# Kernel tuning notes

Hardware: AMD Instinct MI355X
Metric: run time of the kernel (lower is better)

The kernel has to match this reference:

```python
import jax, jax.numpy as jnp
import numpy as np

N = 50000       # nodes
E = 800000      # edges (avg degree 16)
HID = 128       # hidden_size
H = 8           # num_heads
DH = HID // H   # head_dim = 16


def setup_inputs() -> dict:
    key = jax.random.key(0)
    ks = jax.random.split(key, 9)
    wscale = (1.0 / HID) ** 0.5  # ~ torch Linear init scale
    inp = {
        "h": jax.random.normal(ks[0], (N, HID), jnp.float32),
        "val": jnp.ones((E,), jnp.float32),          # A.val (adjacency values)
        "Wq": jax.random.normal(ks[1], (HID, HID), jnp.float32) * wscale,
        "bq": jax.random.normal(ks[2], (HID,), jnp.float32) * wscale,
        "Wk": jax.random.normal(ks[3], (HID, HID), jnp.float32) * wscale,
        "bk": jax.random.normal(ks[4], (HID,), jnp.float32) * wscale,
        "Wv": jax.random.normal(ks[5], (HID, HID), jnp.float32) * wscale,
        "bv": jax.random.normal(ks[6], (HID,), jnp.float32) * wscale,
        "src": jax.random.randint(ks[7], (E,), 0, N, jnp.int32),
        "dst": jax.random.randint(ks[8], (E,), 0, N, jnp.int32),
    }
    return inp


def reference(h, val, Wq, bq, Wk, bk, Wv, bv, src, dst):
    scaling = DH ** (-0.5)
    # projections (torch Linear: x @ W.T + b), reshape (N, head_dim, num_heads)
    q = (h @ Wq.T + bq).reshape(N, DH, H) * scaling
    k = (h @ Wk.T + bk).reshape(N, DH, H)
    v = (h @ Wv.T + bv).reshape(N, DH, H)
    # bsddmm: per-edge per-head scores, masked/scaled by adjacency values
    score = jnp.einsum("edh,edh->eh", q[src], k[dst]) * val[:, None]  # [E, H]
    # sparse per-row softmax (stable, segment-wise over src rows)
    m = jax.ops.segment_max(score, src, num_segments=N)               # [N, H]
    p = jnp.exp(score - m[src])
    s = jax.ops.segment_sum(p, src, num_segments=N)                   # [N, H]
    attn = p / s[src]                                                 # [E, H]
    # bspmm: weighted aggregation of v over edges
    out = jax.ops.segment_sum(attn[:, None, :] * v[dst], src, num_segments=N)  # [N, DH, H]
    return out.reshape(N, HID)
```

## Files before the change

kernel.cpp:

```cpp
#include <hip/hip_runtime.h>
#include <hip/hip_bf16.h>
#include <math.h>

#define HID 128
#define NH  8
#define SCHUNK 512
#define TPAD 136

typedef __attribute__((ext_vector_type(8))) short short8;
typedef __attribute__((ext_vector_type(4))) float f32x4;

static __device__ __forceinline__ float blo(unsigned int u) {
  union { unsigned int i; float f; } c; c.i = u << 16; return c.f;
}
static __device__ __forceinline__ float bhi(unsigned int u) {
  union { unsigned int i; float f; } c; c.i = u & 0xFFFF0000u; return c.f;
}
static __device__ __forceinline__ unsigned short f2bf(float f) {
  union { float f; unsigned int i; } c; c.f = f;
  unsigned int r = c.i + 0x7FFFu + ((c.i >> 16) & 1u);
  return (unsigned short)(r >> 16);
}

__global__ void convert_kernel(const float* __restrict__ src,
                               unsigned short* __restrict__ dst, int n8) {
  int stride = gridDim.x * blockDim.x;
  for (int i = blockIdx.x * blockDim.x + threadIdx.x; i < n8; i += stride) {
    float4 a = ((const float4*)src)[2 * i];
    float4 b = ((const float4*)src)[2 * i + 1];
    uint4 o;
    o.x = ((unsigned int)f2bf(a.y) << 16) | f2bf(a.x);
    o.y = ((unsigned int)f2bf(a.w) << 16) | f2bf(a.z);
    o.z = ((unsigned int)f2bf(b.y) << 16) | f2bf(b.x);
    o.w = ((unsigned int)f2bf(b.w) << 16) | f2bf(b.z);
    ((uint4*)dst)[i] = o;
  }
}

__global__ void convert3_kernel(const float* __restrict__ s0, const float* __restrict__ s1,
                                const float* __restrict__ s2,
                                unsigned short* __restrict__ dst, int n8) {
  const float* s = (blockIdx.y == 0) ? s0 : (blockIdx.y == 1) ? s1 : s2;
  unsigned short* d = dst + (size_t)blockIdx.y * n8 * 8;
  for (int i = blockIdx.x * blockDim.x + threadIdx.x; i < n8;
       i += gridDim.x * blockDim.x) {
    float4 a = ((const float4*)s)[2 * i];
    float4 b = ((const float4*)s)[2 * i + 1];
    uint4 o;
    o.x = ((unsigned int)f2bf(a.y) << 16) | f2bf(a.x);
    o.y = ((unsigned int)f2bf(a.w) << 16) | f2bf(a.z);
    o.z = ((unsigned int)f2bf(b.y) << 16) | f2bf(b.x);
    o.w = ((unsigned int)f2bf(b.w) << 16) | f2bf(b.z);
    ((uint4*)d)[i] = o;
  }
}

__global__ __launch_bounds__(256) void proj_mfma(
    const unsigned short* __restrict__ hb, const unsigned short* __restrict__ wb,
    const float* __restrict__ bq, const float* __restrict__ bk,
    const float* __restrict__ bv,
    unsigned short* __restrict__ qb, unsigned short* __restrict__ kvb, int n) {
  __shared__ unsigned short tile[4][16][TPAD];

  const int y = blockIdx.y;
  const unsigned short* W = wb + (size_t)y * HID * HID;
  const float* bias = (y == 0) ? bq : (y == 1) ? bk : bv;
  const float scale = (y == 0) ? 0.25f : 1.0f;

  unsigned short* out;
  int ostride;
  if (y == 0)      { out = qb;        ostride = HID; }
  else if (y == 1) { out = kvb;       ostride = 2 * HID; }
  else             { out = kvb + HID; ostride = 2 * HID; }

  const int lane = threadIdx.x & 63;
  const int wave = threadIdx.x >> 6;
  const int n0 = blockIdx.x * 64 + wave * 16;

  int arow = n0 + (lane & 15);
  if (arow > n - 1) arow = n - 1;
  const int koff = (lane >> 4) * 8;

  short8 a0 = *(const short8*)(hb + (size_t)arow * HID +  0 + koff);
  short8 a1 = *(const short8*)(hb + (size_t)arow * HID + 32 + koff);
  short8 a2 = *(const short8*)(hb + (size_t)arow * HID + 64 + koff);
  short8 a3 = *(const short8*)(hb + (size_t)arow * HID + 96 + koff);

#pragma unroll
  for (int ct = 0; ct < 8; ++ct) {
    const int c = ct * 16 + (lane & 15);
    const unsigned short* wr = W + (size_t)c * HID + koff;
    f32x4 acc = {0.f, 0.f, 0.f, 0.f};
    acc = __builtin_amdgcn_mfma_f32_16x16x32_bf16(a0, *(const short8*)(wr +  0), acc, 0, 0, 0);
    acc = __builtin_amdgcn_mfma_f32_16x16x32_bf16(a1, *(const short8*)(wr + 32), acc, 0, 0, 0);
    acc = __builtin_amdgcn_mfma_f32_16x16x32_bf16(a2, *(const short8*)(wr + 64), acc, 0, 0, 0);
    acc = __builtin_amdgcn_mfma_f32_16x16x32_bf16(a3, *(const short8*)(wr + 96), acc, 0, 0, 0);

    const float bb = bias[c];
    const int cp = (c & 7) * 16 + (c >> 3);
#pragma unroll
    for (int r = 0; r < 4; ++r) {
      int rl = (lane >> 4) * 4 + r;
      tile[wave][rl][cp] = f2bf((acc[r] + bb) * scale);
    }
  }

#pragma unroll
  for (int p = 0; p < 4; ++p) {
    int rl = p * 4 + (lane >> 4);
    int row = n0 + rl;
    if (row < n) {
      uint4 vv = *(const uint4*)&tile[wave][rl][(lane & 15) * 8];
      *(uint4*)(out + (size_t)row * ostride + (lane & 15) * 8) = vv;
    }
  }
}

__global__ void hist_rank_kernel(const int* __restrict__ src, int* __restrict__ deg,
                                 int* __restrict__ rank, int e) {
  int i = blockIdx.x * blockDim.x + threadIdx.x;
  if (i < e) rank[i] = atomicAdd(&deg[src[i]], 1);
}

__global__ __launch_bounds__(256) void reduce_blocks(
    const int* __restrict__ deg, int* __restrict__ partials, int n) {
  __shared__ int sm[256];
  int base = blockIdx.x * SCHUNK;
  int t = threadIdx.x;
  int i0 = base + t, i1 = base + t + 256;
  int s = ((i0 < n) ? deg[i0] : 0) + ((i1 < n) ? deg[i1] : 0);
  sm[t] = s;
  __syncthreads();
  for (int off = 128; off > 0; off >>= 1) {
    if (t < off) sm[t] += sm[t + off];
    __syncthreads();
  }
  if (t == 0) partials[blockIdx.x] = sm[0];
}

__global__ __launch_bounds__(256) void scan_all(
    const int* __restrict__ deg, const int* __restrict__ partials,
    int* __restrict__ rowptr, int nb, int n) {
  __shared__ int ps[256];
  __shared__ int wsum[4];
  int t = threadIdx.x;
  int pv = (t < nb) ? partials[t] : 0;
  ps[t] = pv;
  __syncthreads();
  for (int off = 1; off < 256; off <<= 1) {
    int u = (t >= off) ? ps[t - off] : 0;
    __syncthreads();
    ps[t] += u;
    __syncthreads();
  }
  const int b = blockIdx.x;
  int myoff = ps[b] - partials[b];
  int total = ps[nb - 1];

  int base = b * SCHUNK;
  int lane = t & 63, wave = t >> 6;
  int i0 = base + 2 * t, i1 = i0 + 1;
  int d0 = (i0 < n) ? deg[i0] : 0;
  int d1 = (i1 < n) ? deg[i1] : 0;
  int s = d0 + d1;
  int incl = s;
#pragma unroll
  for (int off = 1; off < 64; off <<= 1) {
    int u = __shfl_up(incl, off);
    if (lane >= off) incl += u;
  }
  if (lane == 63) wsum[wave] = incl;
  __syncthreads();
  int woff = 0;
  for (int w = 0; w < wave; ++w) woff += wsum[w];
  int excl = woff + (incl - s) + myoff;
  if (i0 < n) rowptr[i0] = excl;
  if (i1 < n) rowptr[i1] = excl + d0;
  if (b == nb - 1 && t == 0) rowptr[n] = total;
}

__global__ void scatter_kernel(const int* __restrict__ src, const int* __restrict__ dst,
                               const float* __restrict__ val, const int* __restrict__ rank,
                               const int* __restrict__ rowptr,
                               unsigned int* __restrict__ csr, int e) {
  int i = blockIdx.x * blockDim.x + threadIdx.x;
  int e2 = e >> 1;
  if (i < e2) {
    int2 s2 = ((const int2*)src)[i];
    int2 d2 = ((const int2*)dst)[i];
    float2 v2 = ((const float2*)val)[i];
    int2 r2 = ((const int2*)rank)[i];
    unsigned int p0 = ((unsigned int)d2.x & 0xFFFFu) | ((unsigned int)f2bf(v2.x) << 16);
    unsigned int p1 = ((unsigned int)d2.y & 0xFFFFu) | ((unsigned int)f2bf(v2.y) << 16);
    csr[rowptr[s2.x] + r2.x] = p0;
    csr[rowptr[s2.y] + r2.y] = p1;
  } else if (i == e2 && (e & 1)) {
    int j = e - 1;
    csr[rowptr[src[j]] + rank[j]] =
        ((unsigned int)dst[j] & 0xFFFFu) | ((unsigned int)f2bf(val[j]) << 16);
  }
}

__global__ __launch_bounds__(256) void node_kernel(
    const unsigned short* __restrict__ qb, const unsigned short* __restrict__ kvb,
    const int* __restrict__ rowptr, const unsigned int* __restrict__ csr,
    float* __restrict__ out, int n) {
  int wid = (blockIdx.x * blockDim.x + threadIdx.x) >> 6;
  int lane = threadIdx.x & 63;
  if (wid >= n) return;
  const int head = lane & 7;
  const int eg = lane >> 3;

  const uint4* qr = (const uint4*)(qb + (size_t)wid * HID + head * 16);
  uint4 q0 = qr[0], q1 = qr[1];
  float qf[16];
  {
    unsigned int qd[8] = {q0.x, q0.y, q0.z, q0.w, q1.x, q1.y, q1.z, q1.w};
#pragma unroll
    for (int j = 0; j < 8; ++j) { qf[2 * j] = blo(qd[j]); qf[2 * j + 1] = bhi(qd[j]); }
  }

  int beg = rowptr[wid], end = rowptr[wid + 1];
  float m = -INFINITY, s = 0.f;
  float o[16];
#pragma unroll
  for (int j = 0; j < 16; ++j) o[j] = 0.f;

  for (int base = beg; base < end; base += 8) {
    int i = base + eg;
    bool valid = i < end;
    unsigned int rec = valid ? csr[i] : 0u;
    int d = rec & 0xFFFFu;
    float vale = bhi(rec);

    const uint4* kr = (const uint4*)(kvb + (size_t)d * (2 * HID) + head * 16);
    uint4 ka = kr[0], kb2 = kr[1];
    uint4 va = kr[16], vb2 = kr[17];

    float dot = 0.f;
    {
      unsigned int kd[8] = {ka.x, ka.y, ka.z, ka.w, kb2.x, kb2.y, kb2.z, kb2.w};
#pragma unroll
      for (int j = 0; j < 8; ++j)
        dot += qf[2 * j] * blo(kd[j]) + qf[2 * j + 1] * bhi(kd[j]);
    }
    float score = valid ? dot * vale : -INFINITY;

    float mx = score;
    mx = fmaxf(mx, __shfl_xor(mx, 8));
    mx = fmaxf(mx, __shfl_xor(mx, 16));
    mx = fmaxf(mx, __shfl_xor(mx, 32));

    if (!__all(mx <= m + 8.f)) {
      float mn = fmaxf(m, mx);
      float c = __expf(m - mn);
      s *= c;
#pragma unroll
      for (int j = 0; j < 16; ++j) o[j] *= c;
      m = mn;
    }

    float w = __expf(score - m);
    s += w;
    {
      unsigned int vd[8] = {va.x, va.y, va.z, va.w, vb2.x, vb2.y, vb2.z, vb2.w};
#pragma unroll
      for (int j = 0; j < 8; ++j) {
        o[2 * j]     += w * blo(vd[j]);
        o[2 * j + 1] += w * bhi(vd[j]);
      }
    }
  }

  s += __shfl_xor(s, 8); s += __shfl_xor(s, 16); s += __shfl_xor(s, 32);
#pragma unroll
  for (int j = 0; j < 16; ++j) {
    o[j] += __shfl_xor(o[j], 8);
    o[j] += __shfl_xor(o[j], 16);
    o[j] += __shfl_xor(o[j], 32);
  }

  float inv = (s > 0.f) ? 1.f / s : 0.f;
#pragma unroll
  for (int dd = 0; dd < 16; ++dd) {
    if (eg == (dd & 7))
      out[(size_t)wid * HID + dd * 8 + head] = o[dd] * inv;
  }
}

extern "C" void kernel_launch(void* const* d_in, const int* in_sizes, int n_in,
                              void* d_out, int out_size, void* d_ws, size_t ws_size,
                              hipStream_t stream) {
  const float* h  = (const float*)d_in[0];
  const float* val = (const float*)d_in[1];
  const float* Wq = (const float*)d_in[2];
  const float* bq = (const float*)d_in[3];
  const float* Wk = (const float*)d_in[4];
  const float* bk = (const float*)d_in[5];
  const float* Wv = (const float*)d_in[6];
  const float* bv = (const float*)d_in[7];
  const int* src  = (const int*)d_in[8];
  const int* dst  = (const int*)d_in[9];

  int N = in_sizes[0] / HID;
  int E = in_sizes[8];
  float* out = (float*)d_out;
  int nb = (N + SCHUNK - 1) / SCHUNK;

  unsigned short* hb  = (unsigned short*)d_ws;
  unsigned short* wb  = hb + (size_t)N * HID;
  unsigned short* qb  = wb + 3 * HID * HID;
  unsigned short* kvb = qb + (size_t)N * HID;
  int* rowptr  = (int*)(kvb + (size_t)2 * N * HID);
  int* deg     = rowptr + (N + 1);
  int* partials = deg + N;
  int* rank    = partials + nb;
  unsigned int* csr = (unsigned int*)(rank + E);

  hipMemsetAsync(deg, 0, sizeof(int) * (size_t)N, stream);

  int n8_h = N * HID / 8;
  convert_kernel<<<(n8_h + 255) / 256, 256, 0, stream>>>(h, hb, n8_h);
  int n8_w = HID * HID / 8;
  convert3_kernel<<<dim3((n8_w + 255) / 256, 3), 256, 0, stream>>>(Wq, Wk, Wv, wb, n8_w);

  proj_mfma<<<dim3((N + 63) / 64, 3), 256, 0, stream>>>(hb, wb, bq, bk, bv, qb, kvb, N);

  hist_rank_kernel<<<(E + 255) / 256, 256, 0, stream>>>(src, deg, rank, E);
  reduce_blocks<<<nb, 256, 0, stream>>>(deg, partials, N);
  scan_all<<<nb, 256, 0, stream>>>(deg, partials, rowptr, nb, N);
  scatter_kernel<<<((E / 2) + 256) / 256, 256, 0, stream>>>(
      src, dst, val, rank, rowptr, csr, E);

  node_kernel<<<(N + 3) / 4, 256, 0, stream>>>(qb, kvb, rowptr, csr, out, N);
}
```

Baseline: 184.2 us.

## Fuse h bf16 conversion into projection and make node kernel grid-stride

Removes the separate h fp32-to-bf16 conversion kernel and its workspace buffer; the projection kernel now loads fp32 h directly and converts in registers. This saves one launch plus a full write and re-read of the bf16 copy, but each of the three projection grid rows now reads fp32 h, doubling read bytes per row. The node kernel becomes a persistent grid-stride loop capped at 2048 blocks, cutting block scheduling overhead at some cost to load balance across varying degrees.

```diff
diff --git a/kernel.cpp b/kernel.cpp
--- a/kernel.cpp
+++ b/kernel.cpp
@@ -22,19 +22,15 @@
   return (unsigned short)(r >> 16);
 }
 
-__global__ void convert_kernel(const float* __restrict__ src,
-                               unsigned short* __restrict__ dst, int n8) {
-  int stride = gridDim.x * blockDim.x;
-  for (int i = blockIdx.x * blockDim.x + threadIdx.x; i < n8; i += stride) {
-    float4 a = ((const float4*)src)[2 * i];
-    float4 b = ((const float4*)src)[2 * i + 1];
-    uint4 o;
-    o.x = ((unsigned int)f2bf(a.y) << 16) | f2bf(a.x);
-    o.y = ((unsigned int)f2bf(a.w) << 16) | f2bf(a.z);
-    o.z = ((unsigned int)f2bf(b.y) << 16) | f2bf(b.x);
-    o.w = ((unsigned int)f2bf(b.w) << 16) | f2bf(b.z);
-    ((uint4*)dst)[i] = o;
-  }
+static __device__ __forceinline__ short8 ldconv8(const float* __restrict__ p) {
+  float4 x = *(const float4*)p;
+  float4 y = *(const float4*)(p + 4);
+  short8 r;
+  r[0] = (short)f2bf(x.x); r[1] = (short)f2bf(x.y);
+  r[2] = (short)f2bf(x.z); r[3] = (short)f2bf(x.w);
+  r[4] = (short)f2bf(y.x); r[5] = (short)f2bf(y.y);
+  r[6] = (short)f2bf(y.z); r[7] = (short)f2bf(y.w);
+  return r;
 }
 
 __global__ void convert3_kernel(const float* __restrict__ s0, const float* __restrict__ s1,
@@ -56,7 +52,7 @@
 }
 
 __global__ __launch_bounds__(256) void proj_mfma(
-    const unsigned short* __restrict__ hb, const unsigned short* __restrict__ wb,
+    const float* __restrict__ h, const unsigned short* __restrict__ wb,
     const float* __restrict__ bq, const float* __restrict__ bk,
     const float* __restrict__ bv,
     unsigned short* __restrict__ qb, unsigned short* __restrict__ kvb, int n) {
@@ -81,10 +77,11 @@
   if (arow > n - 1) arow = n - 1;
   const int koff = (lane >> 4) * 8;
 
-  short8 a0 = *(const short8*)(hb + (size_t)arow * HID +  0 + koff);
-  short8 a1 = *(const short8*)(hb + (size_t)arow * HID + 32 + koff);
-  short8 a2 = *(const short8*)(hb + (size_t)arow * HID + 64 + koff);
-  short8 a3 = *(const short8*)(hb + (size_t)arow * HID + 96 + koff);
+  const float* hr = h + (size_t)arow * HID + koff;
+  short8 a0 = ldconv8(hr +  0);
+  short8 a1 = ldconv8(hr + 32);
+  short8 a2 = ldconv8(hr + 64);
+  short8 a3 = ldconv8(hr + 96);
 
 #pragma unroll
   for (int ct = 0; ct < 8; ++ct) {
@@ -205,86 +202,88 @@
     const unsigned short* __restrict__ qb, const unsigned short* __restrict__ kvb,
     const int* __restrict__ rowptr, const unsigned int* __restrict__ csr,
     float* __restrict__ out, int n) {
-  int wid = (blockIdx.x * blockDim.x + threadIdx.x) >> 6;
-  int lane = threadIdx.x & 63;
-  if (wid >= n) return;
+  const int lane = threadIdx.x & 63;
   const int head = lane & 7;
   const int eg = lane >> 3;
-
-  const uint4* qr = (const uint4*)(qb + (size_t)wid * HID + head * 16);
-  uint4 q0 = qr[0], q1 = qr[1];
-  float qf[16];
-  {
-    unsigned int qd[8] = {q0.x, q0.y, q0.z, q0.w, q1.x, q1.y, q1.z, q1.w};
-#pragma unroll
-    for (int j = 0; j < 8; ++j) { qf[2 * j] = blo(qd[j]); qf[2 * j + 1] = bhi(qd[j]); }
-  }
-
-  int beg = rowptr[wid], end = rowptr[wid + 1];
-  float m = -INFINITY, s = 0.f;
-  float o[16];
-#pragma unroll
-  for (int j = 0; j < 16; ++j) o[j] = 0.f;
-
-  for (int base = beg; base < end; base += 8) {
-    int i = base + eg;
-    bool valid = i < end;
-    unsigned int rec = valid ? csr[i] : 0u;
-    int d = rec & 0xFFFFu;
-    float vale = bhi(rec);
-
-    const uint4* kr = (const uint4*)(kvb + (size_t)d * (2 * HID) + head * 16);
-    uint4 ka = kr[0], kb2 = kr[1];
-    uint4 va = kr[16], vb2 = kr[17];
-
-    float dot = 0.f;
+  const int wave0 = (blockIdx.x * blockDim.x + threadIdx.x) >> 6;
+  const int nwaves = (gridDim.x * blockDim.x) >> 6;
+
+  for (int wid = wave0; wid < n; wid += nwaves) {
+    const uint4* qr = (const uint4*)(qb + (size_t)wid * HID + head * 16);
+    uint4 q0 = qr[0], q1 = qr[1];
+    float qf[16];
     {
-      unsigned int kd[8] = {ka.x, ka.y, ka.z, ka.w, kb2.x, kb2.y, kb2.z, kb2.w};
-#pragma unroll
-      for (int j = 0; j < 8; ++j)
-        dot += qf[2 * j] * blo(kd[j]) + qf[2 * j + 1] * bhi(kd[j]);
-    }
-    float score = valid ? dot * vale : -INFINITY;
-
-    float mx = score;
-    mx = fmaxf(mx, __shfl_xor(mx, 8));
-    mx = fmaxf(mx, __shfl_xor(mx, 16));
-    mx = fmaxf(mx, __shfl_xor(mx, 32));
-
-    if (!__all(mx <= m + 8.f)) {
-      float mn = fmaxf(m, mx);
-      float c = __expf(m - mn);
-      s *= c;
-#pragma unroll
-      for (int j = 0; j < 16; ++j) o[j] *= c;
-      m = mn;
-    }
-
-    float w = __expf(score - m);
-    s += w;
-    {
-      unsigned int vd[8] = {va.x, va.y, va.z, va.w, vb2.x, vb2.y, vb2.z, vb2.w};
-#pragma unroll
-      for (int j = 0; j < 8; ++j) {
-        o[2 * j]     += w * blo(vd[j]);
-        o[2 * j + 1] += w * bhi(vd[j]);
+      unsigned int qd[8] = {q0.x, q0.y, q0.z, q0.w, q1.x, q1.y, q1.z, q1.w};
+#pragma unroll
+      for (int j = 0; j < 8; ++j) { qf[2 * j] = blo(qd[j]); qf[2 * j + 1] = bhi(qd[j]); }
+    }
+
+    int beg = rowptr[wid], end = rowptr[wid + 1];
+    float m = -INFINITY, s = 0.f;
+    float o[16];
+#pragma unroll
+    for (int j = 0; j < 16; ++j) o[j] = 0.f;
+
+    for (int base = beg; base < end; base += 8) {
+      int i = base + eg;
+      bool valid = i < end;
+      unsigned int rec = valid ? csr[i] : 0u;
+      int d = rec & 0xFFFFu;
+      float vale = bhi(rec);
+
+      const uint4* kr = (const uint4*)(kvb + (size_t)d * (2 * HID) + head * 16);
+      uint4 ka = kr[0], kb2 = kr[1];
+      uint4 va = kr[16], vb2 = kr[17];
+
+      float dot = 0.f;
+      {
+        unsigned int kd[8] = {ka.x, ka.y, ka.z, ka.w, kb2.x, kb2.y, kb2.z, kb2.w};
+#pragma unroll
+        for (int j = 0; j < 8; ++j)
+          dot += qf[2 * j] * blo(kd[j]) + qf[2 * j + 1] * bhi(kd[j]);
       }
-    }
-  }
-
-  s += __shfl_xor(s, 8); s += __shfl_xor(s, 16); s += __shfl_xor(s, 32);
-#pragma unroll
-  for (int j = 0; j < 16; ++j) {
-    o[j] += __shfl_xor(o[j], 8);
-    o[j] += __shfl_xor(o[j], 16);
-    o[j] += __shfl_xor(o[j], 32);
-  }
-
-  float inv = (s > 0.f) ? 1.f / s : 0.f;
-#pragma unroll
-  for (int dd = 0; dd < 16; ++dd) {
-    if (eg == (dd & 7))
-      out[(size_t)wid * HID + dd * 8 + head] = o[dd] * inv;
+      float score = valid ? dot * vale : -INFINITY;
+
+      float mx = score;
+      mx = fmaxf(mx, __shfl_xor(mx, 8));
+      mx = fmaxf(mx, __shfl_xor(mx, 16));
+      mx = fmaxf(mx, __shfl_xor(mx, 32));
+
+      if (!__all(mx <= m + 8.f)) {
+        float mn = fmaxf(m, mx);
+        float c = __expf(m - mn);
+        s *= c;
+#pragma unroll
+        for (int j = 0; j < 16; ++j) o[j] *= c;
+        m = mn;
+      }
+
+      float w = __expf(score - m);
+      s += w;
+      {
+        unsigned int vd[8] = {va.x, va.y, va.z, va.w, vb2.x, vb2.y, vb2.z, vb2.w};
+#pragma unroll
+        for (int j = 0; j < 8; ++j) {
+          o[2 * j]     += w * blo(vd[j]);
+          o[2 * j + 1] += w * bhi(vd[j]);
+        }
+      }
+    }
+
+    s += __shfl_xor(s, 8); s += __shfl_xor(s, 16); s += __shfl_xor(s, 32);
+#pragma unroll
+    for (int j = 0; j < 16; ++j) {
+      o[j] += __shfl_xor(o[j], 8);
+      o[j] += __shfl_xor(o[j], 16);
+      o[j] += __shfl_xor(o[j], 32);
+    }
+
+    float inv = (s > 0.f) ? 1.f / s : 0.f;
+#pragma unroll
+    for (int dd = 0; dd < 16; ++dd) {
+      if (eg == (dd & 7))
+        out[(size_t)wid * HID + dd * 8 + head] = o[dd] * inv;
+    }
   }
 }
 
@@ -307,8 +306,7 @@
   float* out = (float*)d_out;
   int nb = (N + SCHUNK - 1) / SCHUNK;
 
-  unsigned short* hb  = (unsigned short*)d_ws;
-  unsigned short* wb  = hb + (size_t)N * HID;
+  unsigned short* wb  = (unsigned short*)d_ws;
   unsigned short* qb  = wb + 3 * HID * HID;
   unsigned short* kvb = qb + (size_t)N * HID;
   int* rowptr  = (int*)(kvb + (size_t)2 * N * HID);
@@ -319,12 +317,10 @@
 
   hipMemsetAsync(deg, 0, sizeof(int) * (size_t)N, stream);
 
-  int n8_h = N * HID / 8;
-  convert_kernel<<<(n8_h + 255) / 256, 256, 0, stream>>>(h, hb, n8_h);
   int n8_w = HID * HID / 8;
   convert3_kernel<<<dim3((n8_w + 255) / 256, 3), 256, 0, stream>>>(Wq, Wk, Wv, wb, n8_w);
 
-  proj_mfma<<<dim3((N + 63) / 64, 3), 256, 0, stream>>>(hb, wb, bq, bk, bv, qb, kvb, N);
+  proj_mfma<<<dim3((N + 63) / 64, 3), 256, 0, stream>>>(h, wb, bq, bk, bv, qb, kvb, N);
 
   hist_rank_kernel<<<(E + 255) / 256, 256, 0, stream>>>(src, deg, rank, E);
   reduce_blocks<<<nb, 256, 0, stream>>>(deg, partials, N);
@@ -332,5 +328,7 @@
   scatter_kernel<<<((E / 2) + 256) / 256, 256, 0, stream>>>(
       src, dst, val, rank, rowptr, csr, E);
 
-  node_kernel<<<(N + 3) / 4, 256, 0, stream>>>(qb, kvb, rowptr, csr, out, N);
-}
+  int nblocks = (N + 3) / 4;
+  if (nblocks > 2048) nblocks = 2048;
+  node_kernel<<<nblocks, 256, 0, stream>>>(qb, kvb, rowptr, csr, out, N);
+}
```

New measurement: 185.8 us. About the same (+0.8%).
